# Performance work log

Hardware: AMD Instinct MI355X
Metric: run time of the kernel (lower is better)

The kernel has to match this reference:

```python
import jax, jax.numpy as jnp
import numpy as np

BT = 64  # chunk size

def _l2norm(x, eps=1e-6):
    n = jnp.linalg.norm(x, axis=-1, keepdims=True)
    return x / jnp.maximum(n, eps)

def _kda_gate(g_raw, A_log, dt_bias):
    # g = -exp(A_log) * softplus(g_raw + dt_bias); broadcast A_log over K
    return -jnp.exp(A_log)[None, None, :, None] * jax.nn.softplus(g_raw.astype(jnp.float32) + dt_bias[None, None].astype(jnp.float32))

def _chunk_kda_fwd(q, k, v, g, beta):
    B, T, H, K = q.shape
    V = v.shape[-1]
    assert T % BT == 0
    NT = T // BT
    scale = K ** -0.5
    q = _l2norm(q.astype(jnp.float32)) * scale
    k = _l2norm(k.astype(jnp.float32))

    def to_chunks(x, d):
        # [B,T,H,d] -> [NT,B,H,BT,d]
        return x.astype(jnp.float32).transpose(0, 2, 1, 3).reshape(B, H, NT, BT, d).transpose(2, 0, 1, 3, 4)

    qc, kc, vc, gc = to_chunks(q, K), to_chunks(k, K), to_chunks(v, V), to_chunks(g, K)
    bc = beta.astype(jnp.float32).transpose(0, 2, 1).reshape(B, H, NT, BT).transpose(2, 0, 1, 3)  # [NT,B,H,BT]

    eye = jnp.eye(BT, dtype=jnp.float32)
    tril_strict = jnp.tril(jnp.ones((BT, BT), bool), -1)
    tril_incl = jnp.tril(jnp.ones((BT, BT), bool), 0)

    def body(S, xs):
        q_i, k_i, v_i, g_i, b_i = xs  # [B,H,BT,*]
        gcum = jnp.cumsum(g_i, axis=-2)                              # [B,H,BT,K]
        diff = gcum[:, :, :, None, :] - gcum[:, :, None, :, :]      # [B,H,BT,BT,K]
        decay = jnp.exp(jnp.minimum(diff, 0.0))
        # intra-chunk k-k matrix, beta row-scaled, strictly lower, negated
        Akk = jnp.einsum('bhik,bhjk,bhijk->bhij', k_i, k_i, decay)
        M = -jnp.where(tril_strict, Akk * b_i[..., :, None], 0.0)
        # UT transform: torch in-place loop solves Tm = (I - M)^{-1}
        Tm = jax.scipy.linalg.solve_triangular(eye - M, jnp.broadcast_to(eye, M.shape), lower=True)
        Afin = Tm * b_i[..., None, :]                                # column scale by beta
        k_eg = k_i * jnp.exp(gcum)
        w = Afin @ k_eg                                              # [B,H,BT,K]
        u = Afin @ v_i                                               # [B,H,BT,V]
        Aqk = jnp.einsum('bhik,bhjk,bhijk->bhij', q_i, k_i, decay)
        Aqk = jnp.where(tril_incl, Aqk, 0.0)
        v_new = u - w @ S
        o_i = (q_i * jnp.exp(gcum)) @ S + Aqk @ v_new
        g_last = gcum[:, :, -1, :]                                   # [B,H,K]
        k_dec = jnp.exp(g_last[:, :, None, :] - gcum) * k_i
        S_new = S * jnp.exp(g_last)[..., None] + jnp.einsum('bhck,bhcv->bhkv', k_dec, v_new)
        return S_new, o_i

    S0 = jnp.zeros((B, H, K, V), jnp.float32)
    _, o = jax.lax.scan(body, S0, (qc, kc, vc, gc, bc))              # o: [NT,B,H,BT,V]
    return o.transpose(1, 2, 0, 3, 4).reshape(B, H, T, V).transpose(0, 2, 1, 3)


def setup_inputs() -> dict:
    key = jax.random.key(0)
    ks = jax.random.split(key, 7)
    B, T, H, K, V = 2, 8192, 16, 32, 64
    return {
        'q': jax.random.normal(ks[0], (B, T, H, K), jnp.float32),
        'k': jax.random.normal(ks[1], (B, T, H, K), jnp.float32),
        'v': jax.random.normal(ks[2], (B, T, H, V), jnp.float32),
        'g_raw': jax.random.normal(ks[3], (B, T, H, K), jnp.float32),
        'beta': jax.random.uniform(ks[4], (B, T, H), jnp.float32),
        'A_log': jax.random.normal(ks[5], (H,), jnp.float32) - 3.0,  # moderate decay rate
        'dt_bias': jax.random.normal(ks[6], (H, K), jnp.float32) * 0.1,
    }


def reference(q, k, v, g_raw, beta, A_log, dt_bias):
    g = _kda_gate(g_raw, A_log, dt_bias)
    return _chunk_kda_fwd(q, k, v, g, beta)
```

## Files before the change

kernel.cpp:

```cpp
#include <hip/hip_runtime.h>
#include <math.h>

#define Tt 8192
#define Hh 16
#define NCH 4096

#define OFF_U   ((size_t)NCH*2048)
#define OFF_M   ((size_t)NCH*6144)
#define OFF_C   ((size_t)NCH*7168)
#define OFF_MS  ((size_t)NCH*9216)
#define OFF_CS  (OFF_MS + (size_t)256*1024)
#define OFF_SS  (OFF_CS + (size_t)256*2048)

__device__ __forceinline__ float softplusf(float x) {
  return fmaxf(x, 0.f) + log1pf(__expf(-fabsf(x)));
}

__global__ __launch_bounds__(256) void kda_phase1(
    const float* __restrict__ kin, const float* __restrict__ vin,
    const float* __restrict__ graw, const float* __restrict__ beta,
    const float* __restrict__ A_log, const float* __restrict__ dt_bias,
    float* __restrict__ ws)
{
  __shared__ float sG[64*33];
  __shared__ float sK[64*33];
  __shared__ float sL[64*64];
  __shared__ float sT[64*65];
  __shared__ float sC[16*17];
  __shared__ float sEgl[32];

  const int tid = threadIdx.x;
  const int ch = blockIdx.x;
  const int c = ch >> 5, bh = ch & 31;
  const int b = bh >> 4, h = bh & 15;
  const int t0 = c*64;
  const int iq = tid >> 2, kq = (tid & 3)*8;

  float* wsW = ws;
  float* wsU = ws + OFF_U;
  float* wsM = ws + OFF_M;
  float* wsCc= ws + OFF_C;

  const float negA = -__expf(A_log[h]);

  {
    const float* gr = graw + (((size_t)b*Tt + t0 + iq)*Hh + h)*32 + kq;
    const float* db = dt_bias + h*32 + kq;
    #pragma unroll
    for (int r = 0; r < 8; ++r)
      sG[iq*33 + kq + r] = negA * softplusf(gr[r] + db[r]);
  }
  __syncthreads();
  if (tid < 32) {
    float acc = 0.f;
    for (int i = 0; i < 64; ++i) { acc += sG[i*33 + tid]; sG[i*33 + tid] = acc; }
  }
  {
    const float* kp = kin + (((size_t)b*Tt + t0 + iq)*Hh + h)*32 + kq;
    float kr[8]; float ss = 0.f;
    #pragma unroll
    for (int r = 0; r < 8; ++r) { kr[r] = kp[r]; ss += kr[r]*kr[r]; }
    ss += __shfl_xor(ss, 1); ss += __shfl_xor(ss, 2);
    const float sc = 1.f / fmaxf(sqrtf(ss), 1e-6f);
    #pragma unroll
    for (int r = 0; r < 8; ++r) sK[iq*33 + kq + r] = kr[r]*sc;
  }
  __syncthreads();

  const float b_cm = beta[((size_t)b*Tt + t0 + (tid & 63))*Hh + h];
  float* P = sT;
  float* Q = sT + 2112;
  for (int jt = 0; jt < 8; ++jt) {
    const int j0 = jt*8;
    #pragma unroll
    for (int r = 0; r < 8; ++r) {
      const int idx = iq*33 + kq + r;
      P[idx] = sK[idx] * __expf(fminf(sG[idx] - sG[j0*33 + kq + r], 0.f));
    }
    {
      const int jj = tid >> 5, kk = tid & 31;
      Q[jj*33 + kk] = sK[(j0+jj)*33 + kk] * __expf(sG[j0*33 + kk] - sG[(j0+jj)*33 + kk]);
    }
    __syncthreads();
    {
      const int i = tid & 63, jj2 = (tid >> 6)*2;
      float a0 = 0.f, a1 = 0.f;
      for (int kk = 0; kk < 32; ++kk) {
        const float p = P[i*33 + kk];
        a0 += p * Q[(jj2  )*33 + kk];
        a1 += p * Q[(jj2+1)*33 + kk];
      }
      const int j_0 = j0 + jj2;
      sL[(j_0  )*64 + i] = (i > j_0  ) ? a0*b_cm : 0.f;
      sL[(j_0+1)*64 + i] = (i > j_0+1) ? a1*b_cm : 0.f;
    }
    __syncthreads();
  }

  for (int e = tid; e < 4096; e += 256) {
    const int row = e >> 6, col = e & 63;
    sT[row*65 + col] = (row == col) ? 1.f : 0.f;
  }
  __syncthreads();
  {
    const int p = tid >> 4, col = tid & 15;
    for (int i = 1; i < 16; ++i) {
      if (tid < 64) {
        const int gi = p*16 + i, gc = p*16 + col;
        float acc = 0.f;
        for (int j = 0; j < i; ++j)
          acc -= sL[(p*16+j)*64 + gi] * sT[(p*16+j)*65 + gc];
        sT[gi*65 + gc] = acc + ((i == col) ? 1.f : 0.f);
      }
      __syncthreads();
    }
  }
  {
    const int ri = tid >> 4, col = tid & 15;
    for (int d = 1; d <= 3; ++d)
      for (int p = d; p < 4; ++p) {
        const int q = p - d;
        float acc = 0.f;
        for (int m = q; m < p; ++m) {
          #pragma unroll
          for (int j = 0; j < 16; ++j)
            acc += sL[(m*16+j)*64 + (p*16+ri)] * sT[(m*16+j)*65 + (q*16+col)];
        }
        sC[ri*17 + col] = acc;
        __syncthreads();
        float acc2 = 0.f;
        #pragma unroll
        for (int j = 0; j < 16; ++j)
          acc2 += sT[(p*16+ri)*65 + (p*16+j)] * sC[j*17 + col];
        sT[(p*16+ri)*65 + (q*16+col)] = -acc2;
        __syncthreads();
      }
  }

  {
    const float b_row = beta[((size_t)b*Tt + t0 + iq)*Hh + h];
    #pragma unroll
    for (int r = 0; r < 8; ++r) {
      const int idx = iq*33 + kq + r;
      const float g = sG[idx], kn = sK[idx];
      sL[idx] = b_row * kn * __expf(g);
      sK[idx] = kn * __expf(sG[63*33 + kq + r] - g);
    }
    if (tid < 32) sEgl[tid] = __expf(sG[63*33 + tid]);
  }
  __syncthreads();

  {
    float acc[8] = {0,0,0,0,0,0,0,0};
    for (int j = 0; j <= iq; ++j) {
      const float t = sT[iq*65 + j];
      #pragma unroll
      for (int r = 0; r < 8; ++r) acc[r] += t * sL[j*33 + kq + r];
    }
    #pragma unroll
    for (int r = 0; r < 8; ++r) {
      wsW[(size_t)ch*2048 + tid*8 + r] = acc[r];
      sG[iq*33 + kq + r] = acc[r];
    }
  }
  __syncthreads();

  {
    #pragma unroll
    for (int r = 0; r < 4; ++r) {
      const int f = tid + 256*r;
      const int j = f >> 4, qd = f & 15;
      const float bj = beta[((size_t)b*Tt + t0 + j)*Hh + h];
      float4 v4 = *(const float4*)(vin + (((size_t)b*Tt + t0 + j)*Hh + h)*64 + qd*4);
      v4.x *= bj; v4.y *= bj; v4.z *= bj; v4.w *= bj;
      *(float4*)(sL + j*64 + qd*4) = v4;
    }
  }
  __syncthreads();

  float uacc[16];
  {
    const int vs = (tid & 3)*16;
    #pragma unroll
    for (int r = 0; r < 16; ++r) uacc[r] = 0.f;
    for (int j = 0; j <= iq; ++j) {
      const float t = sT[iq*65 + j];
      #pragma unroll
      for (int r = 0; r < 16; ++r) uacc[r] += t * sL[j*64 + vs + r];
    }
    #pragma unroll
    for (int r = 0; r < 16; ++r) wsU[(size_t)ch*4096 + tid*16 + r] = uacc[r];
  }
  __syncthreads();
  {
    const int vs = (tid & 3)*16;
    #pragma unroll
    for (int rr = 0; rr < 4; ++rr) {
      float4 o4; o4.x=uacc[rr*4]; o4.y=uacc[rr*4+1]; o4.z=uacc[rr*4+2]; o4.w=uacc[rr*4+3];
      *(float4*)(sL + iq*64 + vs + rr*4) = o4;
    }
  }
  __syncthreads();

  {
    const int a = tid >> 3, b4 = (tid & 7)*4, v8 = (tid & 7)*8;
    float mA[4] = {0,0,0,0};
    float cA[8] = {0,0,0,0,0,0,0,0};
    for (int t = 0; t < 64; ++t) {
      const float kd = sK[t*33 + a];
      #pragma unroll
      for (int r = 0; r < 4; ++r) mA[r] += kd * sG[t*33 + b4 + r];
      #pragma unroll
      for (int r = 0; r < 8; ++r) cA[r] += kd * sL[t*64 + v8 + r];
    }
    float4 m4;
    m4.x = ((a == b4+0) ? sEgl[a] : 0.f) - mA[0];
    m4.y = ((a == b4+1) ? sEgl[a] : 0.f) - mA[1];
    m4.z = ((a == b4+2) ? sEgl[a] : 0.f) - mA[2];
    m4.w = ((a == b4+3) ? sEgl[a] : 0.f) - mA[3];
    *(float4*)(wsM + (size_t)ch*1024 + tid*4) = m4;
    float4 c0, c1;
    c0.x=cA[0]; c0.y=cA[1]; c0.z=cA[2]; c0.w=cA[3];
    c1.x=cA[4]; c1.y=cA[5]; c1.z=cA[6]; c1.w=cA[7];
    *(float4*)(wsCc + (size_t)ch*2048 + tid*8) = c0;
    *(float4*)(wsCc + (size_t)ch*2048 + tid*8 + 4) = c1;
  }
}

__global__ __launch_bounds__(256) void kda_scanA(float* __restrict__ ws)
{
  __shared__ float sMa[32*33];
  __shared__ float sCa[32*64];
  __shared__ float sMc[32*33];
  __shared__ float sCc[32*64];
  const int tid = threadIdx.x;
  const int bh = blockIdx.x >> 3, seg = blockIdx.x & 7;
  const int a = tid >> 3, b4 = (tid & 7)*4, v8 = (tid & 7)*8;
  const float* wsM = ws + OFF_M;
  const float* wsC = ws + OFF_C;

  #pragma unroll
  for (int r = 0; r < 4; ++r) sMa[a*33 + b4 + r] = (a == b4 + r) ? 1.f : 0.f;
  #pragma unroll
  for (int r = 0; r < 8; ++r) sCa[a*64 + v8 + r] = 0.f;
  __syncthreads();

  for (int i = 0; i < 16; ++i) {
    const int ch = (seg*16 + i)*32 + bh;
    float4 m4 = *(const float4*)(wsM + (size_t)ch*1024 + tid*4);
    float4 c0 = *(const float4*)(wsC + (size_t)ch*2048 + tid*8);
    float4 c1 = *(const float4*)(wsC + (size_t)ch*2048 + tid*8 + 4);
    sMc[a*33+b4+0]=m4.x; sMc[a*33+b4+1]=m4.y; sMc[a*33+b4+2]=m4.z; sMc[a*33+b4+3]=m4.w;
    sCc[a*64+v8+0]=c0.x; sCc[a*64+v8+1]=c0.y; sCc[a*64+v8+2]=c0.z; sCc[a*64+v8+3]=c0.w;
    sCc[a*64+v8+4]=c1.x; sCc[a*64+v8+5]=c1.y; sCc[a*64+v8+6]=c1.z; sCc[a*64+v8+7]=c1.w;
    __syncthreads();
    float cn0=0,cn1=0,cn2=0,cn3=0,cn4=0,cn5=0,cn6=0,cn7=0;
    float mn0=0,mn1=0,mn2=0,mn3=0;
    for (int bb = 0; bb < 32; ++bb) {
      const float m = sMc[a*33 + bb];
      const float4 s0 = *(const float4*)(sCa + bb*64 + v8);
      const float4 s1 = *(const float4*)(sCa + bb*64 + v8 + 4);
      cn0 += m*s0.x; cn1 += m*s0.y; cn2 += m*s0.z; cn3 += m*s0.w;
      cn4 += m*s1.x; cn5 += m*s1.y; cn6 += m*s1.z; cn7 += m*s1.w;
      mn0 += m*sMa[bb*33+b4+0]; mn1 += m*sMa[bb*33+b4+1];
      mn2 += m*sMa[bb*33+b4+2]; mn3 += m*sMa[bb*33+b4+3];
    }
    cn0 += sCc[a*64+v8+0]; cn1 += sCc[a*64+v8+1]; cn2 += sCc[a*64+v8+2]; cn3 += sCc[a*64+v8+3];
    cn4 += sCc[a*64+v8+4]; cn5 += sCc[a*64+v8+5]; cn6 += sCc[a*64+v8+6]; cn7 += sCc[a*64+v8+7];
    __syncthreads();
    sCa[a*64+v8+0]=cn0; sCa[a*64+v8+1]=cn1; sCa[a*64+v8+2]=cn2; sCa[a*64+v8+3]=cn3;
    sCa[a*64+v8+4]=cn4; sCa[a*64+v8+5]=cn5; sCa[a*64+v8+6]=cn6; sCa[a*64+v8+7]=cn7;
    sMa[a*33+b4+0]=mn0; sMa[a*33+b4+1]=mn1; sMa[a*33+b4+2]=mn2; sMa[a*33+b4+3]=mn3;
    __syncthreads();
  }
  const size_t sid = (size_t)(bh*8 + seg);
  float* wsMs = ws + OFF_MS;
  float* wsCs = ws + OFF_CS;
  #pragma unroll
  for (int r = 0; r < 4; ++r) wsMs[sid*1024 + tid*4 + r] = sMa[a*33+b4+r];
  #pragma unroll
  for (int r = 0; r < 8; ++r) wsCs[sid*2048 + tid*8 + r] = sCa[a*64+v8+r];
}

__global__ __launch_bounds__(256) void kda_scanB(float* __restrict__ ws)
{
  __shared__ float sS[32*64];
  __shared__ float sM[32*33];
  __shared__ float sC2[32*64];
  const int tid = threadIdx.x;
  const int bh = blockIdx.x;
  const int a = tid >> 3, b4 = (tid & 7)*4, v8 = (tid & 7)*8;
  const float* wsMs = ws + OFF_MS;
  const float* wsCs = ws + OFF_CS;
  float* wsSs = ws + OFF_SS;

  #pragma unroll
  for (int r = 0; r < 8; ++r) sS[a*64 + v8 + r] = 0.f;
  __syncthreads();
  for (int seg = 0; seg < 8; ++seg) {
    const size_t sid = (size_t)(bh*8 + seg);
    #pragma unroll
    for (int r = 0; r < 8; ++r) wsSs[sid*2048 + tid*8 + r] = sS[a*64+v8+r];
    float4 m4 = *(const float4*)(wsMs + sid*1024 + tid*4);
    float4 c0 = *(const float4*)(wsCs + sid*2048 + tid*8);
    float4 c1 = *(const float4*)(wsCs + sid*2048 + tid*8 + 4);
    sM[a*33+b4+0]=m4.x; sM[a*33+b4+1]=m4.y; sM[a*33+b4+2]=m4.z; sM[a*33+b4+3]=m4.w;
    sC2[a*64+v8+0]=c0.x; sC2[a*64+v8+1]=c0.y; sC2[a*64+v8+2]=c0.z; sC2[a*64+v8+3]=c0.w;
    sC2[a*64+v8+4]=c1.x; sC2[a*64+v8+5]=c1.y; sC2[a*64+v8+6]=c1.z; sC2[a*64+v8+7]=c1.w;
    __syncthreads();
    float n0=0,n1=0,n2=0,n3=0,n4=0,n5=0,n6=0,n7=0;
    for (int bb = 0; bb < 32; ++bb) {
      const float m = sM[a*33 + bb];
      const float4 s0 = *(const float4*)(sS + bb*64 + v8);
      const float4 s1 = *(const float4*)(sS + bb*64 + v8 + 4);
      n0 += m*s0.x; n1 += m*s0.y; n2 += m*s0.z; n3 += m*s0.w;
      n4 += m*s1.x; n5 += m*s1.y; n6 += m*s1.z; n7 += m*s1.w;
    }
    n0 += sC2[a*64+v8+0]; n1 += sC2[a*64+v8+1]; n2 += sC2[a*64+v8+2]; n3 += sC2[a*64+v8+3];
    n4 += sC2[a*64+v8+4]; n5 += sC2[a*64+v8+5]; n6 += sC2[a*64+v8+6]; n7 += sC2[a*64+v8+7];
    __syncthreads();
    sS[a*64+v8+0]=n0; sS[a*64+v8+1]=n1; sS[a*64+v8+2]=n2; sS[a*64+v8+3]=n3;
    sS[a*64+v8+4]=n4; sS[a*64+v8+5]=n5; sS[a*64+v8+6]=n6; sS[a*64+v8+7]=n7;
    __syncthreads();
  }
}

__global__ __launch_bounds__(256) void kda_scanC(float* __restrict__ ws)
{
  __shared__ float sS[32*64];
  __shared__ float sW[64*33];
  __shared__ float sM[32*33];
  __shared__ float sC2[32*64];
  const int tid = threadIdx.x;
  const int bh = blockIdx.x >> 3, seg = blockIdx.x & 7;
  const int a = tid >> 3, b4 = (tid & 7)*4, v8 = (tid & 7)*8;
  const int t = tid >> 2, v0 = (tid & 3)*16, kc = (tid & 3)*8;
  float* wsW = ws;
  float* wsU = ws + OFF_U;
  const float* wsM = ws + OFF_M;
  const float* wsC = ws + OFF_C;
  const float* wsSs = ws + OFF_SS;

  const size_t sid = (size_t)(bh*8 + seg);
  #pragma unroll
  for (int r = 0; r < 8; ++r) sS[a*64 + v8 + r] = wsSs[sid*2048 + tid*8 + r];
  __syncthreads();

  for (int i = 0; i < 16; ++i) {
    const int ch = (seg*16 + i)*32 + bh;
    float4 w0 = *(const float4*)(wsW + (size_t)ch*2048 + tid*8);
    float4 w1 = *(const float4*)(wsW + (size_t)ch*2048 + tid*8 + 4);
    sW[t*33+kc+0]=w0.x; sW[t*33+kc+1]=w0.y; sW[t*33+kc+2]=w0.z; sW[t*33+kc+3]=w0.w;
    sW[t*33+kc+4]=w1.x; sW[t*33+kc+5]=w1.y; sW[t*33+kc+6]=w1.z; sW[t*33+kc+7]=w1.w;
    float4 m4 = *(const float4*)(wsM + (size_t)ch*1024 + tid*4);
    float4 c0 = *(const float4*)(wsC + (size_t)ch*2048 + tid*8);
    float4 c1 = *(const float4*)(wsC + (size_t)ch*2048 + tid*8 + 4);
    sM[a*33+b4+0]=m4.x; sM[a*33+b4+1]=m4.y; sM[a*33+b4+2]=m4.z; sM[a*33+b4+3]=m4.w;
    sC2[a*64+v8+0]=c0.x; sC2[a*64+v8+1]=c0.y; sC2[a*64+v8+2]=c0.z; sC2[a*64+v8+3]=c0.w;
    sC2[a*64+v8+4]=c1.x; sC2[a*64+v8+5]=c1.y; sC2[a*64+v8+6]=c1.z; sC2[a*64+v8+7]=c1.w;
    float4 A0 = *(const float4*)(wsU + (size_t)ch*4096 + tid*16);
    float4 A1 = *(const float4*)(wsU + (size_t)ch*4096 + tid*16 + 4);
    float4 A2 = *(const float4*)(wsU + (size_t)ch*4096 + tid*16 + 8);
    float4 A3 = *(const float4*)(wsU + (size_t)ch*4096 + tid*16 + 12);
    __syncthreads();

    for (int bb = 0; bb < 32; ++bb) {
      const float wv = sW[t*33 + bb];
      const float4 s0 = *(const float4*)(sS + bb*64 + v0);
      const float4 s1 = *(const float4*)(sS + bb*64 + v0 + 4);
      const float4 s2 = *(const float4*)(sS + bb*64 + v0 + 8);
      const float4 s3 = *(const float4*)(sS + bb*64 + v0 + 12);
      A0.x -= wv*s0.x; A0.y -= wv*s0.y; A0.z -= wv*s0.z; A0.w -= wv*s0.w;
      A1.x -= wv*s1.x; A1.y -= wv*s1.y; A1.z -= wv*s1.z; A1.w -= wv*s1.w;
      A2.x -= wv*s2.x; A2.y -= wv*s2.y; A2.z -= wv*s2.z; A2.w -= wv*s2.w;
      A3.x -= wv*s3.x; A3.y -= wv*s3.y; A3.z -= wv*s3.z; A3.w -= wv*s3.w;
    }
    *(float4*)(wsU + (size_t)ch*4096 + tid*16)      = A0;
    *(float4*)(wsU + (size_t)ch*4096 + tid*16 + 4)  = A1;
    *(float4*)(wsU + (size_t)ch*4096 + tid*16 + 8)  = A2;
    *(float4*)(wsU + (size_t)ch*4096 + tid*16 + 12) = A3;
    #pragma unroll
    for (int r = 0; r < 8; ++r) wsW[(size_t)ch*2048 + tid*8 + r] = sS[a*64+v8+r];
    float n0=0,n1=0,n2=0,n3=0,n4=0,n5=0,n6=0,n7=0;
    for (int bb = 0; bb < 32; ++bb) {
      const float m = sM[a*33 + bb];
      const float4 s0 = *(const float4*)(sS + bb*64 + v8);
      const float4 s1 = *(const float4*)(sS + bb*64 + v8 + 4);
      n0 += m*s0.x; n1 += m*s0.y; n2 += m*s0.z; n3 += m*s0.w;
      n4 += m*s1.x; n5 += m*s1.y; n6 += m*s1.z; n7 += m*s1.w;
    }
    n0 += sC2[a*64+v8+0]; n1 += sC2[a*64+v8+1]; n2 += sC2[a*64+v8+2]; n3 += sC2[a*64+v8+3];
    n4 += sC2[a*64+v8+4]; n5 += sC2[a*64+v8+5]; n6 += sC2[a*64+v8+6]; n7 += sC2[a*64+v8+7];
    __syncthreads();
    sS[a*64+v8+0]=n0; sS[a*64+v8+1]=n1; sS[a*64+v8+2]=n2; sS[a*64+v8+3]=n3;
    sS[a*64+v8+4]=n4; sS[a*64+v8+5]=n5; sS[a*64+v8+6]=n6; sS[a*64+v8+7]=n7;
    __syncthreads();
  }
}

__global__ __launch_bounds__(256) void kda_phase3(
    const float* __restrict__ qin, const float* __restrict__ kin,
    const float* __restrict__ graw,
    const float* __restrict__ A_log, const float* __restrict__ dt_bias,
    const float* __restrict__ ws, float* __restrict__ out)
{
  __shared__ float sG[64*33];
  __shared__ float sQ[64*33];
  __shared__ float sA[64*65];
  __shared__ float sV[64*64];

  const int tid = threadIdx.x;
  const int ch = blockIdx.x;
  const int c = ch >> 5, bh = ch & 31;
  const int b = bh >> 4, h = bh & 15;
  const int t0 = c*64;
  const int iq = tid >> 2, kq = (tid & 3)*8;

  const float* wsW = ws;
  const float* wsU = ws + OFF_U;

  const float negA = -__expf(A_log[h]);
  {
    const float* gr = graw + (((size_t)b*Tt + t0 + iq)*Hh + h)*32 + kq;
    const float* db = dt_bias + h*32 + kq;
    #pragma unroll
    for (int r = 0; r < 8; ++r)
      sG[iq*33 + kq + r] = negA * softplusf(gr[r] + db[r]);
  }
  __syncthreads();
  if (tid < 32) {
    float acc = 0.f;
    for (int i = 0; i < 64; ++i) { acc += sG[i*33 + tid]; sG[i*33 + tid] = acc; }
  }
  float knr[8];
  {
    const float* qp = qin + (((size_t)b*Tt + t0 + iq)*Hh + h)*32 + kq;
    float qr[8]; float ssq = 0.f;
    #pragma unroll
    for (int r = 0; r < 8; ++r) { qr[r] = qp[r]; ssq += qr[r]*qr[r]; }
    ssq += __shfl_xor(ssq, 1); ssq += __shfl_xor(ssq, 2);
    const float scq = 0.17677669529663687f / fmaxf(sqrtf(ssq), 1e-6f);
    #pragma unroll
    for (int r = 0; r < 8; ++r) sQ[iq*33 + kq + r] = qr[r]*scq;

    const float* kp = kin + (((size_t)b*Tt + t0 + iq)*Hh + h)*32 + kq;
    float ssk = 0.f;
    #pragma unroll
    for (int r = 0; r < 8; ++r) { knr[r] = kp[r]; ssk += knr[r]*knr[r]; }
    ssk += __shfl_xor(ssk, 1); ssk += __shfl_xor(ssk, 2);
    const float sck = 1.f / fmaxf(sqrtf(ssk), 1e-6f);
    #pragma unroll
    for (int r = 0; r < 8; ++r) knr[r] *= sck;
  }
  __syncthreads();

  float* P  = sV;
  float* Qb = sV + 2112;
  for (int jt = 0; jt < 8; ++jt) {
    const int j0 = jt*8;
    #pragma unroll
    for (int r = 0; r < 8; ++r) {
      const int idx = iq*33 + kq + r;
      P[idx] = sQ[idx] * __expf(fminf(sG[idx] - sG[j0*33 + kq + r], 0.f));
    }
    if (iq >= j0 && iq < j0 + 8) {
      const int jj = iq - j0;
      #pragma unroll
      for (int r = 0; r < 8; ++r)
        Qb[jj*33 + kq + r] = knr[r] * __expf(sG[j0*33 + kq + r] - sG[iq*33 + kq + r]);
    }
    __syncthreads();
    {
      const int i = tid & 63, jj2 = (tid >> 6)*2;
      float a0 = 0.f, a1 = 0.f;
      for (int kk = 0; kk < 32; ++kk) {
        const float p = P[i*33 + kk];
        a0 += p * Qb[(jj2  )*33 + kk];
        a1 += p * Qb[(jj2+1)*33 + kk];
      }
      sA[i*65 + j0+jj2  ] = (i >= j0+jj2  ) ? a0 : 0.f;
      sA[i*65 + j0+jj2+1] = (i >= j0+jj2+1) ? a1 : 0.f;
    }
    __syncthreads();
  }
  {
    #pragma unroll
    for (int r = 0; r < 8; ++r) {
      const int idx = iq*33 + kq + r;
      sQ[idx] *= __expf(sG[idx]);
    }
  }
  __syncthreads();
  {
    #pragma unroll
    for (int rr = 0; rr < 2; ++rr) {
      const int f = tid + 256*rr;
      *(float4*)(sG + f*4) = *(const float4*)(wsW + (size_t)ch*2048 + f*4);
    }
    #pragma unroll
    for (int rr = 0; rr < 4; ++rr) {
      const int f = tid + 256*rr;
      *(float4*)(sV + f*4) = *(const float4*)(wsU + (size_t)ch*4096 + f*4);
    }
  }
  __syncthreads();
  {
    const int vs = (tid & 3)*16;
    float acc[16];
    #pragma unroll
    for (int r = 0; r < 16; ++r) acc[r] = 0.f;
    for (int kk = 0; kk < 32; ++kk) {
      const float qv = sQ[iq*33 + kk];
      #pragma unroll
      for (int r = 0; r < 16; ++r) acc[r] += qv * sG[kk*64 + vs + r];
    }
    for (int j = 0; j <= iq; ++j) {
      const float av = sA[iq*65 + j];
      #pragma unroll
      for (int r = 0; r < 16; ++r) acc[r] += av * sV[j*64 + vs + r];
    }
    float* op = out + (((size_t)b*Tt + t0 + iq)*Hh + h)*64 + vs;
    #pragma unroll
    for (int rr = 0; rr < 4; ++rr) {
      float4 o4; o4.x=acc[rr*4]; o4.y=acc[rr*4+1]; o4.z=acc[rr*4+2]; o4.w=acc[rr*4+3];
      *(float4*)(op + rr*4) = o4;
    }
  }
}

extern "C" void kernel_launch(void* const* d_in, const int* in_sizes, int n_in,
                              void* d_out, int out_size, void* d_ws, size_t ws_size,
                              hipStream_t stream) {
  const float* q    = (const float*)d_in[0];
  const float* k    = (const float*)d_in[1];
  const float* v    = (const float*)d_in[2];
  const float* graw = (const float*)d_in[3];
  const float* beta = (const float*)d_in[4];
  const float* A_log= (const float*)d_in[5];
  const float* dtb  = (const float*)d_in[6];
  float* out = (float*)d_out;
  float* ws  = (float*)d_ws;

  kda_phase1<<<NCH, 256, 0, stream>>>(k, v, graw, beta, A_log, dtb, ws);
  kda_scanA<<<256, 256, 0, stream>>>(ws);
  kda_scanB<<<32, 256, 0, stream>>>(ws);
  kda_scanC<<<256, 256, 0, stream>>>(ws);
  kda_phase3<<<NCH, 256, 0, stream>>>(q, k, graw, A_log, dtb, ws, out);
}
```

Before: 615.6 us.

## Move v_new correction into phase3 and split state scans across V tiles

```diff
diff --git a/kernel.cpp b/kernel.cpp
--- a/kernel.cpp
+++ b/kernel.cpp
@@ -26,7 +26,7 @@
   __shared__ float sK[64*33];
   __shared__ float sL[64*64];
   __shared__ float sT[64*65];
-  __shared__ float sC[16*17];
+  __shared__ float sC2[3*272];
   __shared__ float sEgl[32];
 
   const int tid = threadIdx.x;
@@ -68,8 +68,9 @@
   __syncthreads();
 
   const float b_cm = beta[((size_t)b*Tt + t0 + (tid & 63))*Hh + h];
-  float* P = sT;
-  float* Q = sT + 2112;
+  float* P  = sT;
+  float* Qb = sT + 2112;
+  const int i64 = tid & 63, jj2 = (tid >> 6)*2;
   for (int jt = 0; jt < 8; ++jt) {
     const int j0 = jt*8;
     #pragma unroll
@@ -79,21 +80,30 @@
     }
     {
       const int jj = tid >> 5, kk = tid & 31;
-      Q[jj*33 + kk] = sK[(j0+jj)*33 + kk] * __expf(sG[j0*33 + kk] - sG[(j0+jj)*33 + kk]);
-    }
-    __syncthreads();
-    {
-      const int i = tid & 63, jj2 = (tid >> 6)*2;
-      float a0 = 0.f, a1 = 0.f;
-      for (int kk = 0; kk < 32; ++kk) {
-        const float p = P[i*33 + kk];
-        a0 += p * Q[(jj2  )*33 + kk];
-        a1 += p * Q[(jj2+1)*33 + kk];
+      Qb[jj*32 + kk] = sK[(j0+jj)*33 + kk] * __expf(sG[j0*33 + kk] - sG[(j0+jj)*33 + kk]);
+    }
+    __syncthreads();
+    float a0 = 0.f, a1 = 0.f;
+    #pragma unroll
+    for (int hf = 0; hf < 2; ++hf) {
+      const int k0 = hf*16;
+      float qa[16], qb[16];
+      #pragma unroll
+      for (int t4 = 0; t4 < 4; ++t4) {
+        float4 xa = *(const float4*)(Qb + (jj2  )*32 + k0 + t4*4);
+        float4 xb = *(const float4*)(Qb + (jj2+1)*32 + k0 + t4*4);
+        qa[t4*4+0]=xa.x; qa[t4*4+1]=xa.y; qa[t4*4+2]=xa.z; qa[t4*4+3]=xa.w;
+        qb[t4*4+0]=xb.x; qb[t4*4+1]=xb.y; qb[t4*4+2]=xb.z; qb[t4*4+3]=xb.w;
       }
-      const int j_0 = j0 + jj2;
-      sL[(j_0  )*64 + i] = (i > j_0  ) ? a0*b_cm : 0.f;
-      sL[(j_0+1)*64 + i] = (i > j_0+1) ? a1*b_cm : 0.f;
-    }
+      #pragma unroll
+      for (int kk = 0; kk < 16; ++kk) {
+        const float p = P[i64*33 + k0 + kk];
+        a0 += p * qa[kk]; a1 += p * qb[kk];
+      }
+    }
+    const int j_0 = j0 + jj2;
+    sL[(j_0  )*64 + i64] = (i64 > j_0  ) ? a0*b_cm : 0.f;
+    sL[(j_0+1)*64 + i64] = (i64 > j_0+1) ? a1*b_cm : 0.f;
     __syncthreads();
   }
 
@@ -102,40 +112,50 @@
     sT[row*65 + col] = (row == col) ? 1.f : 0.f;
   }
   __syncthreads();
-  {
+  if (tid < 64) {
     const int p = tid >> 4, col = tid & 15;
     for (int i = 1; i < 16; ++i) {
-      if (tid < 64) {
-        const int gi = p*16 + i, gc = p*16 + col;
-        float acc = 0.f;
-        for (int j = 0; j < i; ++j)
-          acc -= sL[(p*16+j)*64 + gi] * sT[(p*16+j)*65 + gc];
-        sT[gi*65 + gc] = acc + ((i == col) ? 1.f : 0.f);
+      const int gi = p*16 + i, gc = p*16 + col;
+      float acc = 0.f;
+      for (int j = 0; j < i; ++j)
+        acc -= sL[(p*16+j)*64 + gi] * sT[(p*16+j)*65 + gc];
+      sT[gi*65 + gc] = acc + ((i == col) ? 1.f : 0.f);
+    }
+  }
+  __syncthreads();
+  {
+    const int wid = tid >> 6;
+    const int lane = tid & 63;
+    const int ri = lane & 15, c4 = (lane >> 4)*4;
+    auto offblk = [&](int p, int q) {
+      float a0=0.f, a1=0.f, a2=0.f, a3=0.f;
+      for (int m = q; m < p; ++m) {
+        #pragma unroll
+        for (int j = 0; j < 16; ++j) {
+          const float lv = sL[(m*16+j)*64 + p*16+ri];
+          const float* tp = sT + (m*16+j)*65 + q*16 + c4;
+          a0 += lv*tp[0]; a1 += lv*tp[1]; a2 += lv*tp[2]; a3 += lv*tp[3];
+        }
       }
-      __syncthreads();
-    }
-  }
-  {
-    const int ri = tid >> 4, col = tid & 15;
-    for (int d = 1; d <= 3; ++d)
-      for (int p = d; p < 4; ++p) {
-        const int q = p - d;
-        float acc = 0.f;
-        for (int m = q; m < p; ++m) {
-          #pragma unroll
-          for (int j = 0; j < 16; ++j)
-            acc += sL[(m*16+j)*64 + (p*16+ri)] * sT[(m*16+j)*65 + (q*16+col)];
-        }
-        sC[ri*17 + col] = acc;
-        __syncthreads();
-        float acc2 = 0.f;
-        #pragma unroll
-        for (int j = 0; j < 16; ++j)
-          acc2 += sT[(p*16+ri)*65 + (p*16+j)] * sC[j*17 + col];
-        sT[(p*16+ri)*65 + (q*16+col)] = -acc2;
-        __syncthreads();
+      float* cp = sC2 + wid*272 + ri*17 + c4;
+      cp[0]=a0; cp[1]=a1; cp[2]=a2; cp[3]=a3;
+      float b0=0.f, b1=0.f, b2=0.f, b3=0.f;
+      #pragma unroll
+      for (int j = 0; j < 16; ++j) {
+        const float tv = sT[(p*16+ri)*65 + p*16 + j];
+        const float* cj = sC2 + wid*272 + j*17 + c4;
+        b0 += tv*cj[0]; b1 += tv*cj[1]; b2 += tv*cj[2]; b3 += tv*cj[3];
       }
-  }
+      float* op = sT + (p*16+ri)*65 + q*16 + c4;
+      op[0]=-b0; op[1]=-b1; op[2]=-b2; op[3]=-b3;
+    };
+    if (wid == 0) offblk(1,0); else if (wid == 1) offblk(2,1); else if (wid == 2) offblk(3,2);
+    __syncthreads();
+    if (wid == 0) offblk(2,0); else if (wid == 1) offblk(3,1);
+    __syncthreads();
+    if (wid == 0) offblk(3,0);
+  }
+  __syncthreads();
 
   {
     const float b_row = beta[((size_t)b*Tt + t0 + iq)*Hh + h];
@@ -143,7 +163,7 @@
     for (int r = 0; r < 8; ++r) {
       const int idx = iq*33 + kq + r;
       const float g = sG[idx], kn = sK[idx];
-      sL[idx] = b_row * kn * __expf(g);
+      sL[iq*32 + kq + r] = b_row * kn * __expf(g);
       sK[idx] = kn * __expf(sG[63*33 + kq + r] - g);
     }
     if (tid < 32) sEgl[tid] = __expf(sG[63*33 + tid]);
@@ -154,13 +174,15 @@
     float acc[8] = {0,0,0,0,0,0,0,0};
     for (int j = 0; j <= iq; ++j) {
       const float t = sT[iq*65 + j];
-      #pragma unroll
-      for (int r = 0; r < 8; ++r) acc[r] += t * sL[j*33 + kq + r];
+      const float4 e0 = *(const float4*)(sL + j*32 + kq);
+      const float4 e1 = *(const float4*)(sL + j*32 + kq + 4);
+      acc[0]+=t*e0.x; acc[1]+=t*e0.y; acc[2]+=t*e0.z; acc[3]+=t*e0.w;
+      acc[4]+=t*e1.x; acc[5]+=t*e1.y; acc[6]+=t*e1.z; acc[7]+=t*e1.w;
     }
     #pragma unroll
     for (int r = 0; r < 8; ++r) {
       wsW[(size_t)ch*2048 + tid*8 + r] = acc[r];
-      sG[iq*33 + kq + r] = acc[r];
+      sG[iq*32 + kq + r] = acc[r];
     }
   }
   __syncthreads();
@@ -185,11 +207,20 @@
     for (int r = 0; r < 16; ++r) uacc[r] = 0.f;
     for (int j = 0; j <= iq; ++j) {
       const float t = sT[iq*65 + j];
-      #pragma unroll
-      for (int r = 0; r < 16; ++r) uacc[r] += t * sL[j*64 + vs + r];
-    }
-    #pragma unroll
-    for (int r = 0; r < 16; ++r) wsU[(size_t)ch*4096 + tid*16 + r] = uacc[r];
+      const float4 e0 = *(const float4*)(sL + j*64 + vs);
+      const float4 e1 = *(const float4*)(sL + j*64 + vs + 4);
+      const float4 e2 = *(const float4*)(sL + j*64 + vs + 8);
+      const float4 e3 = *(const float4*)(sL + j*64 + vs + 12);
+      uacc[0]+=t*e0.x;  uacc[1]+=t*e0.y;  uacc[2]+=t*e0.z;  uacc[3]+=t*e0.w;
+      uacc[4]+=t*e1.x;  uacc[5]+=t*e1.y;  uacc[6]+=t*e1.z;  uacc[7]+=t*e1.w;
+      uacc[8]+=t*e2.x;  uacc[9]+=t*e2.y;  uacc[10]+=t*e2.z; uacc[11]+=t*e2.w;
+      uacc[12]+=t*e3.x; uacc[13]+=t*e3.y; uacc[14]+=t*e3.z; uacc[15]+=t*e3.w;
+    }
+    #pragma unroll
+    for (int rr = 0; rr < 4; ++rr) {
+      float4 o4; o4.x=uacc[rr*4]; o4.y=uacc[rr*4+1]; o4.z=uacc[rr*4+2]; o4.w=uacc[rr*4+3];
+      *(float4*)(wsU + (size_t)ch*4096 + tid*16 + rr*4) = o4;
+    }
   }
   __syncthreads();
   {
@@ -208,10 +239,12 @@
     float cA[8] = {0,0,0,0,0,0,0,0};
     for (int t = 0; t < 64; ++t) {
       const float kd = sK[t*33 + a];
-      #pragma unroll
-      for (int r = 0; r < 4; ++r) mA[r] += kd * sG[t*33 + b4 + r];
-      #pragma unroll
-      for (int r = 0; r < 8; ++r) cA[r] += kd * sL[t*64 + v8 + r];
+      const float4 wv = *(const float4*)(sG + t*32 + b4);
+      mA[0]+=kd*wv.x; mA[1]+=kd*wv.y; mA[2]+=kd*wv.z; mA[3]+=kd*wv.w;
+      const float4 u0 = *(const float4*)(sL + t*64 + v8);
+      const float4 u1 = *(const float4*)(sL + t*64 + v8 + 4);
+      cA[0]+=kd*u0.x; cA[1]+=kd*u0.y; cA[2]+=kd*u0.z; cA[3]+=kd*u0.w;
+      cA[4]+=kd*u1.x; cA[5]+=kd*u1.y; cA[6]+=kd*u1.z; cA[7]+=kd*u1.w;
     }
     float4 m4;
     m4.x = ((a == b4+0) ? sEgl[a] : 0.f) - mA[0];
@@ -230,56 +263,49 @@
 __global__ __launch_bounds__(256) void kda_scanA(float* __restrict__ ws)
 {
   __shared__ float sMa[32*33];
-  __shared__ float sCa[32*64];
   __shared__ float sMc[32*33];
-  __shared__ float sCc[32*64];
+  __shared__ float sCa[32*18];
   const int tid = threadIdx.x;
-  const int bh = blockIdx.x >> 3, seg = blockIdx.x & 7;
-  const int a = tid >> 3, b4 = (tid & 7)*4, v8 = (tid & 7)*8;
+  const int vt = blockIdx.x & 3, seg = (blockIdx.x >> 2) & 7, bh = blockIdx.x >> 5;
+  const int v0 = vt*16;
+  const int a = tid >> 3, b4 = (tid & 7)*4, c2 = (tid & 7)*2;
   const float* wsM = ws + OFF_M;
   const float* wsC = ws + OFF_C;
 
   #pragma unroll
   for (int r = 0; r < 4; ++r) sMa[a*33 + b4 + r] = (a == b4 + r) ? 1.f : 0.f;
-  #pragma unroll
-  for (int r = 0; r < 8; ++r) sCa[a*64 + v8 + r] = 0.f;
+  sCa[a*18 + c2] = 0.f; sCa[a*18 + c2 + 1] = 0.f;
   __syncthreads();
 
   for (int i = 0; i < 16; ++i) {
     const int ch = (seg*16 + i)*32 + bh;
     float4 m4 = *(const float4*)(wsM + (size_t)ch*1024 + tid*4);
-    float4 c0 = *(const float4*)(wsC + (size_t)ch*2048 + tid*8);
-    float4 c1 = *(const float4*)(wsC + (size_t)ch*2048 + tid*8 + 4);
+    float2 cc = *(const float2*)(wsC + (size_t)ch*2048 + a*64 + v0 + c2);
     sMc[a*33+b4+0]=m4.x; sMc[a*33+b4+1]=m4.y; sMc[a*33+b4+2]=m4.z; sMc[a*33+b4+3]=m4.w;
-    sCc[a*64+v8+0]=c0.x; sCc[a*64+v8+1]=c0.y; sCc[a*64+v8+2]=c0.z; sCc[a*64+v8+3]=c0.w;
-    sCc[a*64+v8+4]=c1.x; sCc[a*64+v8+5]=c1.y; sCc[a*64+v8+6]=c1.z; sCc[a*64+v8+7]=c1.w;
-    __syncthreads();
-    float cn0=0,cn1=0,cn2=0,cn3=0,cn4=0,cn5=0,cn6=0,cn7=0;
-    float mn0=0,mn1=0,mn2=0,mn3=0;
+    __syncthreads();
+    float cn0 = cc.x, cn1 = cc.y;
+    float mn0=0.f, mn1=0.f, mn2=0.f, mn3=0.f;
     for (int bb = 0; bb < 32; ++bb) {
       const float m = sMc[a*33 + bb];
-      const float4 s0 = *(const float4*)(sCa + bb*64 + v8);
-      const float4 s1 = *(const float4*)(sCa + bb*64 + v8 + 4);
-      cn0 += m*s0.x; cn1 += m*s0.y; cn2 += m*s0.z; cn3 += m*s0.w;
-      cn4 += m*s1.x; cn5 += m*s1.y; cn6 += m*s1.z; cn7 += m*s1.w;
+      const float2 s2 = *(const float2*)(sCa + bb*18 + c2);
+      cn0 += m*s2.x; cn1 += m*s2.y;
       mn0 += m*sMa[bb*33+b4+0]; mn1 += m*sMa[bb*33+b4+1];
       mn2 += m*sMa[bb*33+b4+2]; mn3 += m*sMa[bb*33+b4+3];
     }
-    cn0 += sCc[a*64+v8+0]; cn1 += sCc[a*64+v8+1]; cn2 += sCc[a*64+v8+2]; cn3 += sCc[a*64+v8+3];
-    cn4 += sCc[a*64+v8+4]; cn5 += sCc[a*64+v8+5]; cn6 += sCc[a*64+v8+6]; cn7 += sCc[a*64+v8+7];
-    __syncthreads();
-    sCa[a*64+v8+0]=cn0; sCa[a*64+v8+1]=cn1; sCa[a*64+v8+2]=cn2; sCa[a*64+v8+3]=cn3;
-    sCa[a*64+v8+4]=cn4; sCa[a*64+v8+5]=cn5; sCa[a*64+v8+6]=cn6; sCa[a*64+v8+7]=cn7;
+    __syncthreads();
+    sCa[a*18+c2] = cn0; sCa[a*18+c2+1] = cn1;
     sMa[a*33+b4+0]=mn0; sMa[a*33+b4+1]=mn1; sMa[a*33+b4+2]=mn2; sMa[a*33+b4+3]=mn3;
     __syncthreads();
   }
   const size_t sid = (size_t)(bh*8 + seg);
   float* wsMs = ws + OFF_MS;
   float* wsCs = ws + OFF_CS;
-  #pragma unroll
-  for (int r = 0; r < 4; ++r) wsMs[sid*1024 + tid*4 + r] = sMa[a*33+b4+r];
-  #pragma unroll
-  for (int r = 0; r < 8; ++r) wsCs[sid*2048 + tid*8 + r] = sCa[a*64+v8+r];
+  if (vt == 0) {
+    #pragma unroll
+    for (int r = 0; r < 4; ++r) wsMs[sid*1024 + tid*4 + r] = sMa[a*33+b4+r];
+  }
+  float2 co; co.x = sCa[a*18+c2]; co.y = sCa[a*18+c2+1];
+  *(float2*)(wsCs + sid*2048 + a*64 + v0 + c2) = co;
 }
 
 __global__ __launch_bounds__(256) void kda_scanB(float* __restrict__ ws)
@@ -327,73 +353,39 @@
 
 __global__ __launch_bounds__(256) void kda_scanC(float* __restrict__ ws)
 {
-  __shared__ float sS[32*64];
-  __shared__ float sW[64*33];
   __shared__ float sM[32*33];
-  __shared__ float sC2[32*64];
+  __shared__ float sS[32*18];
   const int tid = threadIdx.x;
-  const int bh = blockIdx.x >> 3, seg = blockIdx.x & 7;
-  const int a = tid >> 3, b4 = (tid & 7)*4, v8 = (tid & 7)*8;
-  const int t = tid >> 2, v0 = (tid & 3)*16, kc = (tid & 3)*8;
-  float* wsW = ws;
-  float* wsU = ws + OFF_U;
+  const int vt = blockIdx.x & 3, seg = (blockIdx.x >> 2) & 7, bh = blockIdx.x >> 5;
+  const int v0 = vt*16;
+  const int a = tid >> 3, b4 = (tid & 7)*4, c2 = (tid & 7)*2;
   const float* wsM = ws + OFF_M;
-  const float* wsC = ws + OFF_C;
+  float* wsC = ws + OFF_C;
   const float* wsSs = ws + OFF_SS;
 
   const size_t sid = (size_t)(bh*8 + seg);
-  #pragma unroll
-  for (int r = 0; r < 8; ++r) sS[a*64 + v8 + r] = wsSs[sid*2048 + tid*8 + r];
+  {
+    float2 s0 = *(const float2*)(wsSs + sid*2048 + a*64 + v0 + c2);
+    sS[a*18 + c2] = s0.x; sS[a*18 + c2 + 1] = s0.y;
+  }
   __syncthreads();
 
   for (int i = 0; i < 16; ++i) {
     const int ch = (seg*16 + i)*32 + bh;
-    float4 w0 = *(const float4*)(wsW + (size_t)ch*2048 + tid*8);
-    float4 w1 = *(const float4*)(wsW + (size_t)ch*2048 + tid*8 + 4);
-    sW[t*33+kc+0]=w0.x; sW[t*33+kc+1]=w0.y; sW[t*33+kc+2]=w0.z; sW[t*33+kc+3]=w0.w;
-    sW[t*33+kc+4]=w1.x; sW[t*33+kc+5]=w1.y; sW[t*33+kc+6]=w1.z; sW[t*33+kc+7]=w1.w;
     float4 m4 = *(const float4*)(wsM + (size_t)ch*1024 + tid*4);
-    float4 c0 = *(const float4*)(wsC + (size_t)ch*2048 + tid*8);
-    float4 c1 = *(const float4*)(wsC + (size_t)ch*2048 + tid*8 + 4);
+    float2 cc = *(const float2*)(wsC + (size_t)ch*2048 + a*64 + v0 + c2);
     sM[a*33+b4+0]=m4.x; sM[a*33+b4+1]=m4.y; sM[a*33+b4+2]=m4.z; sM[a*33+b4+3]=m4.w;
-    sC2[a*64+v8+0]=c0.x; sC2[a*64+v8+1]=c0.y; sC2[a*64+v8+2]=c0.z; sC2[a*64+v8+3]=c0.w;
-    sC2[a*64+v8+4]=c1.x; sC2[a*64+v8+5]=c1.y; sC2[a*64+v8+6]=c1.z; sC2[a*64+v8+7]=c1.w;
-    float4 A0 = *(const float4*)(wsU + (size_t)ch*4096 + tid*16);
-    float4 A1 = *(const float4*)(wsU + (size_t)ch*4096 + tid*16 + 4);
-    float4 A2 = *(const float4*)(wsU + (size_t)ch*4096 + tid*16 + 8);
-    float4 A3 = *(const float4*)(wsU + (size_t)ch*4096 + tid*16 + 12);
-    __syncthreads();
-
-    for (int bb = 0; bb < 32; ++bb) {
-      const float wv = sW[t*33 + bb];
-      const float4 s0 = *(const float4*)(sS + bb*64 + v0);
-      const float4 s1 = *(const float4*)(sS + bb*64 + v0 + 4);
-      const float4 s2 = *(const float4*)(sS + bb*64 + v0 + 8);
-      const float4 s3 = *(const float4*)(sS + bb*64 + v0 + 12);
-      A0.x -= wv*s0.x; A0.y -= wv*s0.y; A0.z -= wv*s0.z; A0.w -= wv*s0.w;
-      A1.x -= wv*s1.x; A1.y -= wv*s1.y; A1.z -= wv*s1.z; A1.w -= wv*s1.w;
-      A2.x -= wv*s2.x; A2.y -= wv*s2.y; A2.z -= wv*s2.z; A2.w -= wv*s2.w;
-      A3.x -= wv*s3.x; A3.y -= wv*s3.y; A3.z -= wv*s3.z; A3.w -= wv*s3.w;
-    }
-    *(float4*)(wsU + (size_t)ch*4096 + tid*16)      = A0;
-    *(float4*)(wsU + (size_t)ch*4096 + tid*16 + 4)  = A1;
-    *(float4*)(wsU + (size_t)ch*4096 + tid*16 + 8)  = A2;
-    *(float4*)(wsU + (size_t)ch*4096 + tid*16 + 12) = A3;
-    #pragma unroll
-    for (int r = 0; r < 8; ++r) wsW[(size_t)ch*2048 + tid*8 + r] = sS[a*64+v8+r];
-    float n0=0,n1=0,n2=0,n3=0,n4=0,n5=0,n6=0,n7=0;
+    float2 se; se.x = sS[a*18+c2]; se.y = sS[a*18+c2+1];
+    *(float2*)(wsC + (size_t)ch*2048 + a*64 + v0 + c2) = se;
+    __syncthreads();
+    float n0 = cc.x, n1 = cc.y;
     for (int bb = 0; bb < 32; ++bb) {
       const float m = sM[a*33 + bb];
-      const float4 s0 = *(const float4*)(sS + bb*64 + v8);
-      const float4 s1 = *(const float4*)(sS + bb*64 + v8 + 4);
-      n0 += m*s0.x; n1 += m*s0.y; n2 += m*s0.z; n3 += m*s0.w;
-      n4 += m*s1.x; n5 += m*s1.y; n6 += m*s1.z; n7 += m*s1.w;
-    }
-    n0 += sC2[a*64+v8+0]; n1 += sC2[a*64+v8+1]; n2 += sC2[a*64+v8+2]; n3 += sC2[a*64+v8+3];
-    n4 += sC2[a*64+v8+4]; n5 += sC2[a*64+v8+5]; n6 += sC2[a*64+v8+6]; n7 += sC2[a*64+v8+7];
-    __syncthreads();
-    sS[a*64+v8+0]=n0; sS[a*64+v8+1]=n1; sS[a*64+v8+2]=n2; sS[a*64+v8+3]=n3;
-    sS[a*64+v8+4]=n4; sS[a*64+v8+5]=n5; sS[a*64+v8+6]=n6; sS[a*64+v8+7]=n7;
+      const float2 s2 = *(const float2*)(sS + bb*18 + c2);
+      n0 += m*s2.x; n1 += m*s2.y;
+    }
+    __syncthreads();
+    sS[a*18+c2] = n0; sS[a*18+c2+1] = n1;
     __syncthreads();
   }
 }
@@ -418,6 +410,7 @@
 
   const float* wsW = ws;
   const float* wsU = ws + OFF_U;
+  const float* wsS = ws + OFF_C;
 
   const float negA = -__expf(A_log[h]);
   {
@@ -456,6 +449,7 @@
 
   float* P  = sV;
   float* Qb = sV + 2112;
+  const int i64 = tid & 63, jj2 = (tid >> 6)*2;
   for (int jt = 0; jt < 8; ++jt) {
     const int j0 = jt*8;
     #pragma unroll
@@ -467,27 +461,39 @@
       const int jj = iq - j0;
       #pragma unroll
       for (int r = 0; r < 8; ++r)
-        Qb[jj*33 + kq + r] = knr[r] * __expf(sG[j0*33 + kq + r] - sG[iq*33 + kq + r]);
-    }
-    __syncthreads();
-    {
-      const int i = tid & 63, jj2 = (tid >> 6)*2;
-      float a0 = 0.f, a1 = 0.f;
-      for (int kk = 0; kk < 32; ++kk) {
-        const float p = P[i*33 + kk];
-        a0 += p * Qb[(jj2  )*33 + kk];
-        a1 += p * Qb[(jj2+1)*33 + kk];
+        Qb[jj*32 + kq + r] = knr[r] * __expf(sG[j0*33 + kq + r] - sG[iq*33 + kq + r]);
+    }
+    __syncthreads();
+    float a0 = 0.f, a1 = 0.f;
+    #pragma unroll
+    for (int hf = 0; hf < 2; ++hf) {
+      const int k0 = hf*16;
+      float qa[16], qb[16];
+      #pragma unroll
+      for (int t4 = 0; t4 < 4; ++t4) {
+        float4 xa = *(const float4*)(Qb + (jj2  )*32 + k0 + t4*4);
+        float4 xb = *(const float4*)(Qb + (jj2+1)*32 + k0 + t4*4);
+        qa[t4*4+0]=xa.x; qa[t4*4+1]=xa.y; qa[t4*4+2]=xa.z; qa[t4*4+3]=xa.w;
+        qb[t4*4+0]=xb.x; qb[t4*4+1]=xb.y; qb[t4*4+2]=xb.z; qb[t4*4+3]=xb.w;
       }
-      sA[i*65 + j0+jj2  ] = (i >= j0+jj2  ) ? a0 : 0.f;
-      sA[i*65 + j0+jj2+1] = (i >= j0+jj2+1) ? a1 : 0.f;
-    }
-    __syncthreads();
-  }
+      #pragma unroll
+      for (int kk = 0; kk < 16; ++kk) {
+        const float p = P[i64*33 + k0 + kk];
+        a0 += p * qa[kk]; a1 += p * qb[kk];
+      }
+    }
+    const int j_0 = j0 + jj2;
+    sA[i64*65 + j_0  ] = (i64 >= j_0  ) ? a0 : 0.f;
+    sA[i64*65 + j_0+1] = (i64 >= j_0+1) ? a1 : 0.f;
+    __syncthreads();
+  }
+
+  float qgr[8];
   {
     #pragma unroll
     for (int r = 0; r < 8; ++r) {
       const int idx = iq*33 + kq + r;
-      sQ[idx] *= __expf(sG[idx]);
+      qgr[r] = sQ[idx] * __expf(sG[idx]);
     }
   }
   __syncthreads();
@@ -495,8 +501,28 @@
     #pragma unroll
     for (int rr = 0; rr < 2; ++rr) {
       const int f = tid + 256*rr;
-      *(float4*)(sG + f*4) = *(const float4*)(wsW + (size_t)ch*2048 + f*4);
-    }
+      *(float4*)(sG + f*4) = *(const float4*)(wsS + (size_t)ch*2048 + f*4);
+    }
+    *(float4*)(sV + tid*8)     = *(const float4*)(wsW + (size_t)ch*2048 + tid*8);
+    *(float4*)(sV + tid*8 + 4) = *(const float4*)(wsW + (size_t)ch*2048 + tid*8 + 4);
+  }
+  __syncthreads();
+  {
+    float qe[8];
+    #pragma unroll
+    for (int r = 0; r < 8; ++r) qe[r] = qgr[r];
+    for (int j = 0; j <= iq; ++j) {
+      const float av = sA[iq*65 + j];
+      const float4 w0 = *(const float4*)(sV + j*32 + kq);
+      const float4 w1 = *(const float4*)(sV + j*32 + kq + 4);
+      qe[0]-=av*w0.x; qe[1]-=av*w0.y; qe[2]-=av*w0.z; qe[3]-=av*w0.w;
+      qe[4]-=av*w1.x; qe[5]-=av*w1.y; qe[6]-=av*w1.z; qe[7]-=av*w1.w;
+    }
+    #pragma unroll
+    for (int r = 0; r < 8; ++r) sQ[iq*33 + kq + r] = qe[r];
+  }
+  __syncthreads();
+  {
     #pragma unroll
     for (int rr = 0; rr < 4; ++rr) {
       const int f = tid + 256*rr;
@@ -511,13 +537,25 @@
     for (int r = 0; r < 16; ++r) acc[r] = 0.f;
     for (int kk = 0; kk < 32; ++kk) {
       const float qv = sQ[iq*33 + kk];
-      #pragma unroll
-      for (int r = 0; r < 16; ++r) acc[r] += qv * sG[kk*64 + vs + r];
+      const float4 s0 = *(const float4*)(sG + kk*64 + vs);
+      const float4 s1 = *(const float4*)(sG + kk*64 + vs + 4);
+      const float4 s2 = *(const float4*)(sG + kk*64 + vs + 8);
+      const float4 s3 = *(const float4*)(sG + kk*64 + vs + 12);
+      acc[0]+=qv*s0.x;  acc[1]+=qv*s0.y;  acc[2]+=qv*s0.z;  acc[3]+=qv*s0.w;
+      acc[4]+=qv*s1.x;  acc[5]+=qv*s1.y;  acc[6]+=qv*s1.z;  acc[7]+=qv*s1.w;
+      acc[8]+=qv*s2.x;  acc[9]+=qv*s2.y;  acc[10]+=qv*s2.z; acc[11]+=qv*s2.w;
+      acc[12]+=qv*s3.x; acc[13]+=qv*s3.y; acc[14]+=qv*s3.z; acc[15]+=qv*s3.w;
     }
     for (int j = 0; j <= iq; ++j) {
       const float av = sA[iq*65 + j];
-      #pragma unroll
-      for (int r = 0; r < 16; ++r) acc[r] += av * sV[j*64 + vs + r];
+      const float4 u0 = *(const float4*)(sV + j*64 + vs);
+      const float4 u1 = *(const float4*)(sV + j*64 + vs + 4);
+      const float4 u2 = *(const float4*)(sV + j*64 + vs + 8);
+      const float4 u3 = *(const float4*)(sV + j*64 + vs + 12);
+      acc[0]+=av*u0.x;  acc[1]+=av*u0.y;  acc[2]+=av*u0.z;  acc[3]+=av*u0.w;
+      acc[4]+=av*u1.x;  acc[5]+=av*u1.y;  acc[6]+=av*u1.z;  acc[7]+=av*u1.w;
+      acc[8]+=av*u2.x;  acc[9]+=av*u2.y;  acc[10]+=av*u2.z; acc[11]+=av*u2.w;
+      acc[12]+=av*u3.x; acc[13]+=av*u3.y; acc[14]+=av*u3.z; acc[15]+=av*u3.w;
     }
     float* op = out + (((size_t)b*Tt + t0 + iq)*Hh + h)*64 + vs;
     #pragma unroll
@@ -542,8 +580,8 @@
   float* ws  = (float*)d_ws;
 
   kda_phase1<<<NCH, 256, 0, stream>>>(k, v, graw, beta, A_log, dtb, ws);
-  kda_scanA<<<256, 256, 0, stream>>>(ws);
+  kda_scanA<<<1024, 256, 0, stream>>>(ws);
   kda_scanB<<<32, 256, 0, stream>>>(ws);
-  kda_scanC<<<256, 256, 0, stream>>>(ws);
+  kda_scanC<<<1024, 256, 0, stream>>>(ws);
   kda_phase3<<<NCH, 256, 0, stream>>>(q, k, graw, A_log, dtb, ws, out);
 }
```

Result: faster. 572.7 us (-7.0%).
